# Performance work log

Measured on AMD Instinct MI355X. Metric: run time of the kernel, lower is better.

The kernel has to match this reference:

```python
import jax, jax.numpy as jnp
import numpy as np

N_NODES = 50000
N_EDGES = 800000
N_GRAPHS = 256
D = 256
L = 3
BN_EPS = 1e-5


def setup_inputs() -> dict:
    key = jax.random.key(0)
    ks = jax.random.split(key, 8)
    x = jax.random.normal(ks[0], (N_NODES, D), dtype=jnp.float32)
    edge_index = jax.random.randint(ks[1], (2, N_EDGES), 0, N_NODES, dtype=jnp.int64)
    batch = jnp.sort(jax.random.randint(ks[2], (N_NODES,), 0, N_GRAPHS, dtype=jnp.int64))
    # small init scale keeps ReLU/BN chain numerically tame
    w1 = jax.random.normal(ks[3], (L, D, D), dtype=jnp.float32) * 0.05
    b1 = jnp.zeros((L, D), dtype=jnp.float32)
    w2 = jax.random.normal(ks[4], (L, D, D), dtype=jnp.float32) * 0.05
    b2 = jnp.zeros((L, D), dtype=jnp.float32)
    gamma = jnp.ones((L, D), dtype=jnp.float32)
    beta = jnp.zeros((L, D), dtype=jnp.float32)
    return {"x": x, "edge_index": edge_index, "batch": batch,
            "w1": w1, "b1": b1, "w2": w2, "b2": b2,
            "gamma": gamma, "beta": beta}


def reference(x, edge_index, batch, w1, b1, w2, b2, gamma, beta):
    src = edge_index[0]  # message senders (x_j)
    dst = edge_index[1]  # aggregation targets (x_i)
    h = x
    xs = []
    for i in range(L):
        # GINConv (eps=0): MLP(x_i + sum_{j in N(i)} x_j)
        agg = jax.ops.segment_sum(h[src], dst, num_segments=N_NODES)  # [N, D]
        z = h + agg
        z = jnp.maximum(z @ w1[i] + b1[i], 0.0) @ w2[i] + b2[i]  # Linear-ReLU-Linear
        z = jnp.maximum(z, 0.0)  # F.relu after conv
        # BatchNorm1d (training mode: biased batch stats over nodes)
        mean = jnp.mean(z, axis=0)
        var = jnp.var(z, axis=0)
        z = (z - mean) * jax.lax.rsqrt(var + BN_EPS) * gamma[i] + beta[i]
        xs.append(z)
        h = z
    # global_add_pool per layer, then concat along features -> [G, L*D]
    pooled = [jax.ops.segment_sum(xi, batch, num_segments=N_GRAPHS) for xi in xs]
    return jnp.concatenate(pooled, axis=1)
```

## Files before the change

kernel.cpp:

```cpp
#include <hip/hip_runtime.h>

#define NN 50000
#define NE 800000
#define NG 256
#define DD 256
#define NL 3
#define BN_EPS 1e-5f
#define MPAD 50048
#define CAP 96
#define NMB 391

typedef short bf16x8 __attribute__((ext_vector_type(8)));
typedef float f32x4 __attribute__((ext_vector_type(4)));
typedef unsigned short ushort8 __attribute__((ext_vector_type(8)));

__device__ __forceinline__ unsigned short f2bf(float f) {
    unsigned int u = __float_as_uint(f);
    u += 0x7FFFu + ((u >> 16) & 1u);
    return (unsigned short)(u >> 16);
}
__device__ __forceinline__ float bf2f(unsigned short s) {
    return __uint_as_float(((unsigned int)s) << 16);
}

#define R0 3200000
#define R1 393216
#define R2 50000
#define R3 12288
#define R4 256
#define R5 256
#define RTOT (R0 + R1 + R2 + R3 + R4 + R5)

__global__ void k_setup(const float* __restrict__ x, const float* __restrict__ w1,
                        const float* __restrict__ w2, const int* __restrict__ batch,
                        unsigned short* __restrict__ hbf, unsigned short* __restrict__ wt,
                        int* __restrict__ deg, unsigned short* __restrict__ zbf,
                        int* __restrict__ gstart) {
    int i = blockIdx.x * blockDim.x + threadIdx.x;
    if (i < R0) {
        float4 v = ((const float4*)x)[i];
        ushort4 o;
        o.x = f2bf(v.x); o.y = f2bf(v.y); o.z = f2bf(v.z); o.w = f2bf(v.w);
        ((ushort4*)hbf)[i] = o;
        return;
    }
    i -= R0;
    if (i < R1) {
        int mat = i >> 16;
        int n = (i >> 8) & 255;
        int k = i & 255;
        const float* src = (mat < 3) ? (w1 + ((size_t)mat << 16)) : (w2 + ((size_t)(mat - 3) << 16));
        wt[i] = f2bf(src[k * 256 + n]);
        return;
    }
    i -= R1;
    if (i < R2) { deg[i] = 0; return; }
    i -= R2;
    if (i < R3) { zbf[NN * DD + i] = 0; return; }
    i -= R3;
    if (i < R4) { hbf[(size_t)NN * DD + i] = 0; return; }
    i -= R4;
    if (i < R5) {
        int g = i;
        int lo = 0, hi = NN;
        while (lo < hi) {
            int mid = (lo + hi) >> 1;
            if (batch[mid] < g) lo = mid + 1; else hi = mid;
        }
        gstart[g] = lo;
        if (g == 0) gstart[NG] = NN;
    }
}

__global__ void k_scatter(const int* __restrict__ ei, int* __restrict__ deg,
                          unsigned short* __restrict__ elist) {
    int e = blockIdx.x * blockDim.x + threadIdx.x;
    if (e >= NE) return;
    int s = ei[e];
    int d = ei[NE + e];
    int pos = atomicAdd(&deg[d], 1);
    elist[(size_t)d * CAP + pos] = (unsigned short)s;
}

template<int HALF>
__global__ __launch_bounds__(256) void k_agg_bf(const unsigned short* __restrict__ h,
                                                const int* __restrict__ deg,
                                                const unsigned short* __restrict__ elist,
                                                unsigned short* __restrict__ z0) {
    int wave = threadIdx.x >> 6;
    int lane = threadIdx.x & 63;
    int node = blockIdx.x * 4 + wave;
    int chunk = lane & 15;
    int eway = lane >> 4;
    const int base = HALF * 16 + chunk;
    const ushort8* h8 = (const ushort8*)h;

    float acc[8];
    if (eway == 0) {
        ushort8 own = h8[(size_t)node * 32 + base];
        #pragma unroll
        for (int j = 0; j < 8; ++j) acc[j] = bf2f(own[j]);
    } else {
        #pragma unroll
        for (int j = 0; j < 8; ++j) acc[j] = 0.f;
    }

    int n = deg[node];
    const unsigned short* el = elist + (size_t)node * CAP;
    int i = 0;
    for (; i + 8 <= n; i += 8) {
        ushort8 sv = *(const ushort8*)(el + i);
        int i0 = sv[eway];
        int i1 = sv[eway + 4];
        ushort8 r0 = h8[(size_t)i0 * 32 + base];
        ushort8 r1 = h8[(size_t)i1 * 32 + base];
        #pragma unroll
        for (int j = 0; j < 8; ++j) acc[j] += bf2f(r0[j]);
        #pragma unroll
        for (int j = 0; j < 8; ++j) acc[j] += bf2f(r1[j]);
    }
    for (; i < n; i += 4) {
        int e = i + eway;
        int idx = (e < n) ? (int)el[e] : NN;
        ushort8 r = h8[(size_t)idx * 32 + base];
        #pragma unroll
        for (int j = 0; j < 8; ++j) acc[j] += bf2f(r[j]);
    }

    ushort8 o;
    #pragma unroll
    for (int j = 0; j < 8; ++j) {
        float v = acc[j];
        v += __shfl_xor(v, 16);
        v += __shfl_xor(v, 32);
        o[j] = f2bf(v);
    }
    if (eway == 0) ((ushort8*)z0)[(size_t)node * 32 + base] = o;
}

__global__ __launch_bounds__(512, 2) void k_mlp(const unsigned short* __restrict__ A,
                                                const unsigned short* __restrict__ BT1,
                                                const unsigned short* __restrict__ BT2,
                                                const float* __restrict__ b1,
                                                const float* __restrict__ b2,
                                                float* __restrict__ Cout,
                                                float* __restrict__ pstat) {
    __shared__ short As[128 * 64];
    __shared__ short Bs[256 * 64];
    __shared__ short H1[128 * 256];
    __shared__ float spart[2][256][2];
    int tid = threadIdx.x;
    int lane = tid & 63;
    int wave = tid >> 6;
    int wr = wave >> 2, wc = wave & 3;
    long m0 = (long)blockIdx.x * 128;
    const int r = lane & 15, hi = lane >> 4;

    f32x4 acc[4][4];
    #pragma unroll
    for (int m = 0; m < 4; ++m)
        #pragma unroll
        for (int n = 0; n < 4; ++n)
            acc[m][n] = (f32x4){0.f, 0.f, 0.f, 0.f};

    for (int k0 = 0; k0 < DD; k0 += 64) {
        #pragma unroll
        for (int p = 0; p < 2; ++p) {
            int flat = p * 512 + tid;
            int row = flat >> 3, c8 = flat & 7;
            int slot = c8 ^ (row & 7);
            *(bf16x8*)(As + row * 64 + slot * 8) =
                *(const bf16x8*)(A + (m0 + row) * DD + k0 + c8 * 8);
        }
        #pragma unroll
        for (int p = 0; p < 4; ++p) {
            int flat = p * 512 + tid;
            int row = flat >> 3, c8 = flat & 7;
            int slot = c8 ^ (row & 7);
            *(bf16x8*)(Bs + row * 64 + slot * 8) =
                *(const bf16x8*)(BT1 + (long)row * DD + k0 + c8 * 8);
        }
        __syncthreads();
        bf16x8 af[4][2], bfr[4][2];
        #pragma unroll
        for (int m = 0; m < 4; ++m) {
            int row = wr * 64 + m * 16 + r;
            #pragma unroll
            for (int kk = 0; kk < 2; ++kk) {
                int slot = (kk * 4 + hi) ^ (row & 7);
                af[m][kk] = *(const bf16x8*)(As + row * 64 + slot * 8);
            }
        }
        #pragma unroll
        for (int n = 0; n < 4; ++n) {
            int col = wc * 64 + n * 16 + r;
            #pragma unroll
            for (int kk = 0; kk < 2; ++kk) {
                int slot = (kk * 4 + hi) ^ (col & 7);
                bfr[n][kk] = *(const bf16x8*)(Bs + col * 64 + slot * 8);
            }
        }
        #pragma unroll
        for (int kk = 0; kk < 2; ++kk)
            #pragma unroll
            for (int m = 0; m < 4; ++m)
                #pragma unroll
                for (int n = 0; n < 4; ++n)
                    acc[m][n] = __builtin_amdgcn_mfma_f32_16x16x32_bf16(af[m][kk], bfr[n][kk], acc[m][n], 0, 0, 0);
        __syncthreads();
    }

    #pragma unroll
    for (int n = 0; n < 4; ++n) {
        int col = wc * 64 + n * 16 + r;
        float bv = b1[col];
        int g = col >> 3, j8 = col & 7;
        #pragma unroll
        for (int m = 0; m < 4; ++m) {
            #pragma unroll
            for (int j = 0; j < 4; ++j) {
                int row = wr * 64 + m * 16 + hi * 4 + j;
                float v = acc[m][n][j] + bv;
                v = v > 0.f ? v : 0.f;
                H1[row * 256 + (g ^ (row & 7)) * 8 + j8] = (short)f2bf(v);
            }
        }
    }
    #pragma unroll
    for (int m = 0; m < 4; ++m)
        #pragma unroll
        for (int n = 0; n < 4; ++n)
            acc[m][n] = (f32x4){0.f, 0.f, 0.f, 0.f};
    __syncthreads();

    for (int k0 = 0; k0 < DD; k0 += 64) {
        #pragma unroll
        for (int p = 0; p < 4; ++p) {
            int flat = p * 512 + tid;
            int row = flat >> 3, c8 = flat & 7;
            int slot = c8 ^ (row & 7);
            *(bf16x8*)(Bs + row * 64 + slot * 8) =
                *(const bf16x8*)(BT2 + (long)row * DD + k0 + c8 * 8);
        }
        __syncthreads();
        bf16x8 af[4][2], bfr[4][2];
        #pragma unroll
        for (int m = 0; m < 4; ++m) {
            int row = wr * 64 + m * 16 + r;
            #pragma unroll
            for (int kk = 0; kk < 2; ++kk) {
                int g = (k0 >> 3) + kk * 4 + hi;
                af[m][kk] = *(const bf16x8*)(H1 + row * 256 + (g ^ (row & 7)) * 8);
            }
        }
        #pragma unroll
        for (int n = 0; n < 4; ++n) {
            int col = wc * 64 + n * 16 + r;
            #pragma unroll
            for (int kk = 0; kk < 2; ++kk) {
                int slot = (kk * 4 + hi) ^ (col & 7);
                bfr[n][kk] = *(const bf16x8*)(Bs + col * 64 + slot * 8);
            }
        }
        #pragma unroll
        for (int kk = 0; kk < 2; ++kk)
            #pragma unroll
            for (int m = 0; m < 4; ++m)
                #pragma unroll
                for (int n = 0; n < 4; ++n)
                    acc[m][n] = __builtin_amdgcn_mfma_f32_16x16x32_bf16(af[m][kk], bfr[n][kk], acc[m][n], 0, 0, 0);
        __syncthreads();
    }

    #pragma unroll
    for (int n = 0; n < 4; ++n) {
        int col = wc * 64 + n * 16 + r;
        float bv = b2[col];
        float cs = 0.f, cs2 = 0.f;
        #pragma unroll
        for (int m = 0; m < 4; ++m) {
            #pragma unroll
            for (int j = 0; j < 4; ++j) {
                long grow = m0 + wr * 64 + m * 16 + hi * 4 + j;
                float v = acc[m][n][j] + bv;
                v = v > 0.f ? v : 0.f;
                Cout[grow * DD + col] = v;
                float vm = (grow < NN) ? v : 0.f;
                cs += vm; cs2 += vm * vm;
            }
        }
        cs  += __shfl_xor(cs, 16);  cs  += __shfl_xor(cs, 32);
        cs2 += __shfl_xor(cs2, 16); cs2 += __shfl_xor(cs2, 32);
        if (hi == 0) {
            spart[wr][col][0] = cs;
            spart[wr][col][1] = cs2;
        }
    }
    __syncthreads();
    if (tid < 256) {
        float s  = spart[0][tid][0] + spart[1][tid][0];
        float s2 = spart[0][tid][1] + spart[1][tid][1];
        pstat[(size_t)blockIdx.x * 512 + tid] = s;
        pstat[(size_t)blockIdx.x * 512 + 256 + tid] = s2;
    }
}

__global__ __launch_bounds__(256) void k_bnscale2(const float* __restrict__ pstat,
                                                  const float* __restrict__ gamma,
                                                  const float* __restrict__ beta,
                                                  float* __restrict__ ss) {
    int c = blockIdx.x;
    int t = threadIdx.x;
    float s = 0.f, s2 = 0.f;
    for (int mb = t; mb < NMB; mb += 256) {
        s  += pstat[(size_t)mb * 512 + c];
        s2 += pstat[(size_t)mb * 512 + 256 + c];
    }
    __shared__ float rs[256], rs2[256];
    rs[t] = s; rs2[t] = s2;
    __syncthreads();
    #pragma unroll
    for (int d = 128; d > 0; d >>= 1) {
        if (t < d) { rs[t] += rs[t + d]; rs2[t] += rs2[t + d]; }
        __syncthreads();
    }
    if (t == 0) {
        float mean = rs[0] * (1.0f / NN);
        float var = rs2[0] * (1.0f / NN) - mean * mean;
        float sc = gamma[c] * rsqrtf(var + BN_EPS);
        ss[c] = sc;
        ss[DD + c] = beta[c] - mean * sc;
    }
}

template<int LAST>
__global__ __launch_bounds__(512) void k_bnpool(const float* __restrict__ z,
                                                const float* __restrict__ ss,
                                                const int* __restrict__ gstart,
                                                unsigned short* __restrict__ hbf,
                                                float* __restrict__ out, int layer) {
    __shared__ float4 red[16][32];
    int g = blockIdx.x;
    int ch = blockIdx.y;
    int t = threadIdx.x;
    int q = t & 31, rg = t >> 5;
    int cq = ch * 32 + q;
    float4 sc = ((const float4*)ss)[cq];
    float4 sh = ((const float4*)(ss + DD))[cq];
    int lo = gstart[g], hi = gstart[g + 1];
    float4 s = {0.f, 0.f, 0.f, 0.f};
    const float4* z4 = (const float4*)z;
    ushort4* h4 = (ushort4*)hbf;
    for (int r = lo + rg; r < hi; r += 16) {
        float4 v = z4[(size_t)r * 64 + cq];
        v.x = v.x * sc.x + sh.x;
        v.y = v.y * sc.y + sh.y;
        v.z = v.z * sc.z + sh.z;
        v.w = v.w * sc.w + sh.w;
        s.x += v.x; s.y += v.y; s.z += v.z; s.w += v.w;
        if (!LAST) {
            ushort4 o;
            o.x = f2bf(v.x); o.y = f2bf(v.y); o.z = f2bf(v.z); o.w = f2bf(v.w);
            h4[(size_t)r * 64 + cq] = o;
        }
    }
    red[rg][q] = s;
    __syncthreads();
    #pragma unroll
    for (int d = 8; d > 0; d >>= 1) {
        if (rg < d) {
            float4 a = red[rg][q], b = red[rg + d][q];
            a.x += b.x; a.y += b.y; a.z += b.z; a.w += b.w;
            red[rg][q] = a;
        }
        __syncthreads();
    }
    if (rg == 0) {
        ((float4*)(out + (size_t)g * (NL * DD) + layer * DD))[cq] = red[0][q];
    }
}

extern "C" void kernel_launch(void* const* d_in, const int* in_sizes, int n_in,
                              void* d_out, int out_size, void* d_ws, size_t ws_size,
                              hipStream_t stream) {
    const float* x     = (const float*)d_in[0];
    const int*   ei    = (const int*)d_in[1];
    const int*   batch = (const int*)d_in[2];
    const float* w1    = (const float*)d_in[3];
    const float* b1    = (const float*)d_in[4];
    const float* w2    = (const float*)d_in[5];
    const float* b2    = (const float*)d_in[6];
    const float* gamma = (const float*)d_in[7];
    const float* beta  = (const float*)d_in[8];
    float* out = (float*)d_out;

    char* ws = (char*)d_ws;
    size_t off = 0;
    auto alloc = [&](size_t bytes) -> void* {
        void* p = ws + off;
        off += (bytes + 255) & ~size_t(255);
        return p;
    };
    float*          buf0 = (float*)alloc((size_t)MPAD * DD * 4);
    unsigned short* zbf  = (unsigned short*)alloc((size_t)MPAD * DD * 2);
    unsigned short* hbf  = (unsigned short*)alloc((size_t)(NN + 64) * DD * 2);
    unsigned short* wt   = (unsigned short*)alloc((size_t)6 * DD * DD * 2);
    int* deg    = (int*)alloc((size_t)NN * 4);
    unsigned short* elist = (unsigned short*)alloc((size_t)NN * CAP * 2);
    int* gstart = (int*)alloc((size_t)(NG + 1) * 4);
    float* pstat = (float*)alloc((size_t)NMB * 512 * 4);
    float* ss   = (float*)alloc(2 * DD * 4);

    k_setup<<<(RTOT + 255) / 256, 256, 0, stream>>>(x, w1, w2, batch, hbf, wt, deg, zbf, gstart);
    k_scatter<<<(NE + 255) / 256, 256, 0, stream>>>(ei, deg, elist);

    for (int l = 0; l < NL; ++l) {
        k_agg_bf<0><<<NN / 4, 256, 0, stream>>>(hbf, deg, elist, zbf);
        k_agg_bf<1><<<NN / 4, 256, 0, stream>>>(hbf, deg, elist, zbf);
        k_mlp<<<NMB, 512, 0, stream>>>(zbf, wt + (size_t)l * DD * DD,
                                       wt + (size_t)(3 + l) * DD * DD,
                                       b1 + l * DD, b2 + l * DD, buf0, pstat);
        k_bnscale2<<<DD, 256, 0, stream>>>(pstat, gamma + l * DD, beta + l * DD, ss);
        if (l < NL - 1)
            k_bnpool<0><<<dim3(NG, 2), 512, 0, stream>>>(buf0, ss, gstart, hbf, out, l);
        else
            k_bnpool<1><<<dim3(NG, 2), 512, 0, stream>>>(buf0, ss, gstart, hbf, out, l);
    }
}
```

Before: 416.5 us.

## Bin edges by destination block and merge aggregation halves into one kernel

Replaces the global-atomic edge scatter with a three-pass binning scheme: histogram destinations into 256-node bins, scan, write packed edges into bins, then build per-node edge lists using shared-memory atomics. This is meant to cut contended global atomics and scattered writes. The aggregation also becomes a single launch covering the full 256-wide row, with two half-waves each taking alternate edges, instead of two launches over 128-column halves. The price is extra kernels and a binbuf buffer. Each wave now processes twice the row width per edge, so every gather fetches whole rows.

```diff
diff --git a/kernel.cpp b/kernel.cpp
--- a/kernel.cpp
+++ b/kernel.cpp
@@ -9,6 +9,7 @@
 #define MPAD 50048
 #define CAP 96
 #define NMB 391
+#define NBIN 196
 
 typedef short bf16x8 __attribute__((ext_vector_type(8)));
 typedef float f32x4 __attribute__((ext_vector_type(4)));
@@ -25,17 +26,17 @@
 
 #define R0 3200000
 #define R1 393216
-#define R2 50000
-#define R3 12288
+#define R2 12288
+#define R3 256
 #define R4 256
-#define R5 256
+#define R5 NBIN
 #define RTOT (R0 + R1 + R2 + R3 + R4 + R5)
 
 __global__ void k_setup(const float* __restrict__ x, const float* __restrict__ w1,
                         const float* __restrict__ w2, const int* __restrict__ batch,
                         unsigned short* __restrict__ hbf, unsigned short* __restrict__ wt,
-                        int* __restrict__ deg, unsigned short* __restrict__ zbf,
-                        int* __restrict__ gstart) {
+                        unsigned short* __restrict__ zbf, int* __restrict__ gstart,
+                        int* __restrict__ bin_cnt) {
     int i = blockIdx.x * blockDim.x + threadIdx.x;
     if (i < R0) {
         float4 v = ((const float4*)x)[i];
@@ -54,13 +55,11 @@
         return;
     }
     i -= R1;
-    if (i < R2) { deg[i] = 0; return; }
+    if (i < R2) { zbf[NN * DD + i] = 0; return; }
     i -= R2;
-    if (i < R3) { zbf[NN * DD + i] = 0; return; }
+    if (i < R3) { hbf[(size_t)NN * DD + i] = 0; return; }
     i -= R3;
-    if (i < R4) { hbf[(size_t)NN * DD + i] = 0; return; }
-    i -= R4;
-    if (i < R5) {
+    if (i < R4) {
         int g = i;
         int lo = 0, hi = NN;
         while (lo < hi) {
@@ -69,20 +68,99 @@
         }
         gstart[g] = lo;
         if (g == 0) gstart[NG] = NN;
-    }
-}
-
-__global__ void k_scatter(const int* __restrict__ ei, int* __restrict__ deg,
-                          unsigned short* __restrict__ elist) {
-    int e = blockIdx.x * blockDim.x + threadIdx.x;
-    if (e >= NE) return;
-    int s = ei[e];
-    int d = ei[NE + e];
-    int pos = atomicAdd(&deg[d], 1);
-    elist[(size_t)d * CAP + pos] = (unsigned short)s;
-}
-
-template<int HALF>
+        return;
+    }
+    i -= R4;
+    if (i < R5) bin_cnt[i] = 0;
+}
+
+__global__ __launch_bounds__(256) void k_bin1(const int* __restrict__ ei,
+                                              int* __restrict__ bin_cnt) {
+    __shared__ int hist[NBIN];
+    int t = threadIdx.x;
+    for (int i = t; i < NBIN; i += 256) hist[i] = 0;
+    __syncthreads();
+    #pragma unroll
+    for (int j = 0; j < 4; ++j) {
+        int e = blockIdx.x * 1024 + j * 256 + t;
+        if (e < NE) atomicAdd(&hist[ei[NE + e] >> 8], 1);
+    }
+    __syncthreads();
+    for (int i = t; i < NBIN; i += 256)
+        if (hist[i]) atomicAdd(&bin_cnt[i], hist[i]);
+}
+
+__global__ void k_binscan(const int* __restrict__ bin_cnt, int* __restrict__ bin_start,
+                          int* __restrict__ bin_cursor) {
+    __shared__ int s[256];
+    int t = threadIdx.x;
+    int v = (t < NBIN) ? bin_cnt[t] : 0;
+    s[t] = v;
+    __syncthreads();
+    #pragma unroll
+    for (int d = 1; d < 256; d <<= 1) {
+        int a = (t >= d) ? s[t - d] : 0;
+        __syncthreads();
+        s[t] += a;
+        __syncthreads();
+    }
+    int excl = s[t] - v;
+    if (t < NBIN) { bin_start[t] = excl; bin_cursor[t] = excl; }
+    if (t == 0) bin_start[NBIN] = NE;
+}
+
+__global__ __launch_bounds__(256) void k_bin2(const int* __restrict__ ei,
+                                              int* __restrict__ bin_cursor,
+                                              unsigned int* __restrict__ binbuf) {
+    __shared__ int hist[NBIN], base[NBIN], lcur[NBIN];
+    int t = threadIdx.x;
+    for (int i = t; i < NBIN; i += 256) { hist[i] = 0; lcur[i] = 0; }
+    __syncthreads();
+    int d[4], s[4];
+    #pragma unroll
+    for (int j = 0; j < 4; ++j) {
+        int e = blockIdx.x * 1024 + j * 256 + t;
+        if (e < NE) {
+            s[j] = ei[e];
+            d[j] = ei[NE + e];
+            atomicAdd(&hist[d[j] >> 8], 1);
+        } else d[j] = -1;
+    }
+    __syncthreads();
+    for (int i = t; i < NBIN; i += 256)
+        base[i] = hist[i] ? atomicAdd(&bin_cursor[i], hist[i]) : 0;
+    __syncthreads();
+    #pragma unroll
+    for (int j = 0; j < 4; ++j) {
+        if (d[j] >= 0) {
+            int b = d[j] >> 8;
+            int o = atomicAdd(&lcur[b], 1);
+            binbuf[base[b] + o] = (unsigned)s[j] | ((unsigned)(d[j] & 255) << 16);
+        }
+    }
+}
+
+__global__ __launch_bounds__(256) void k_bin3(const unsigned int* __restrict__ binbuf,
+                                              const int* __restrict__ bin_start,
+                                              unsigned short* __restrict__ elist,
+                                              int* __restrict__ deg) {
+    __shared__ int ldeg[256];
+    int b = blockIdx.x, t = threadIdx.x;
+    ldeg[t] = 0;
+    __syncthreads();
+    int lo = bin_start[b], hi = bin_start[b + 1];
+    for (int i = lo + t; i < hi; i += 256) {
+        unsigned v = binbuf[i];
+        int src = v & 0xFFFF;
+        int dl = v >> 16;
+        int pos = atomicAdd(&ldeg[dl], 1);
+        elist[(size_t)(b * 256 + dl) * CAP + pos] = (unsigned short)src;
+    }
+    __syncthreads();
+    int node = b * 256 + t;
+    if (node < NN) deg[node] = ldeg[t];
+}
+
 __global__ __launch_bounds__(256) void k_agg_bf(const unsigned short* __restrict__ h,
                                                 const int* __restrict__ deg,
                                                 const unsigned short* __restrict__ elist,
@@ -90,14 +168,13 @@
     int wave = threadIdx.x >> 6;
     int lane = threadIdx.x & 63;
     int node = blockIdx.x * 4 + wave;
-    int chunk = lane & 15;
-    int eway = lane >> 4;
-    const int base = HALF * 16 + chunk;
+    int chunk = lane & 31;
+    int half = lane >> 5;
     const ushort8* h8 = (const ushort8*)h;
 
     float acc[8];
-    if (eway == 0) {
-        ushort8 own = h8[(size_t)node * 32 + base];
+    if (half == 0) {
+        ushort8 own = h8[(size_t)node * 32 + chunk];
         #pragma unroll
         for (int j = 0; j < 8; ++j) acc[j] = bf2f(own[j]);
     } else {
@@ -110,19 +187,28 @@
     int i = 0;
     for (; i + 8 <= n; i += 8) {
         ushort8 sv = *(const ushort8*)(el + i);
-        int i0 = sv[eway];
-        int i1 = sv[eway + 4];
-        ushort8 r0 = h8[(size_t)i0 * 32 + base];
-        ushort8 r1 = h8[(size_t)i1 * 32 + base];
+        int i0 = half ? sv[1] : sv[0];
+        int i1 = half ? sv[3] : sv[2];
+        int i2 = half ? sv[5] : sv[4];
+        int i3 = half ? sv[7] : sv[6];
+        ushort8 r0 = h8[(size_t)i0 * 32 + chunk];
+        ushort8 r1 = h8[(size_t)i1 * 32 + chunk];
+        ushort8 r2 = h8[(size_t)i2 * 32 + chunk];
+        ushort8 r3 = h8[(size_t)i3 * 32 + chunk];
         #pragma unroll
         for (int j = 0; j < 8; ++j) acc[j] += bf2f(r0[j]);
         #pragma unroll
         for (int j = 0; j < 8; ++j) acc[j] += bf2f(r1[j]);
-    }
-    for (; i < n; i += 4) {
-        int e = i + eway;
-        int idx = (e < n) ? (int)el[e] : NN;
-        ushort8 r = h8[(size_t)idx * 32 + base];
+        #pragma unroll
+        for (int j = 0; j < 8; ++j) acc[j] += bf2f(r2[j]);
+        #pragma unroll
+        for (int j = 0; j < 8; ++j) acc[j] += bf2f(r3[j]);
+    }
+    for (; i < n; i += 2) {
+        int s0 = el[i];
+        int s1 = (i + 1 < n) ? (int)el[i + 1] : NN;
+        int idx = half ? s1 : s0;
+        ushort8 r = h8[(size_t)idx * 32 + chunk];
         #pragma unroll
         for (int j = 0; j < 8; ++j) acc[j] += bf2f(r[j]);
     }
@@ -130,12 +216,10 @@
     ushort8 o;
     #pragma unroll
     for (int j = 0; j < 8; ++j) {
-        float v = acc[j];
-        v += __shfl_xor(v, 16);
-        v += __shfl_xor(v, 32);
-        o[j] = f2bf(v);
-    }
-    if (eway == 0) ((ushort8*)z0)[(size_t)node * 32 + base] = o;
+        float other = __shfl_xor(acc[j], 32);
+        o[j] = f2bf(acc[j] + other);
+    }
+    if (half == 0) ((ushort8*)z0)[(size_t)node * 32 + chunk] = o;
 }
 
 __global__ __launch_bounds__(512, 2) void k_mlp(const unsigned short* __restrict__ A,
@@ -407,16 +491,23 @@
     unsigned short* wt   = (unsigned short*)alloc((size_t)6 * DD * DD * 2);
     int* deg    = (int*)alloc((size_t)NN * 4);
     unsigned short* elist = (unsigned short*)alloc((size_t)NN * CAP * 2);
+    unsigned int* binbuf = (unsigned int*)alloc((size_t)NE * 4);
+    int* bin_cnt    = (int*)alloc(NBIN * 4);
+    int* bin_start  = (int*)alloc((NBIN + 1) * 4);
+    int* bin_cursor = (int*)alloc(NBIN * 4);
     int* gstart = (int*)alloc((size_t)(NG + 1) * 4);
     float* pstat = (float*)alloc((size_t)NMB * 512 * 4);
     float* ss   = (float*)alloc(2 * DD * 4);
 
-    k_setup<<<(RTOT + 255) / 256, 256, 0, stream>>>(x, w1, w2, batch, hbf, wt, deg, zbf, gstart);
-    k_scatter<<<(NE + 255) / 256, 256, 0, stream>>>(ei, deg, elist);
+    k_setup<<<(RTOT + 255) / 256, 256, 0, stream>>>(x, w1, w2, batch, hbf, wt, zbf, gstart, bin_cnt);
+    const int EB = (NE + 1023) / 1024;
+    k_bin1<<<EB, 256, 0, stream>>>(ei, bin_cnt);
+    k_binscan<<<1, 256, 0, stream>>>(bin_cnt, bin_start, bin_cursor);
+    k_bin2<<<EB, 256, 0, stream>>>(ei, bin_cursor, binbuf);
+    k_bin3<<<NBIN, 256, 0, stream>>>(binbuf, bin_start, elist, deg);
 
     for (int l = 0; l < NL; ++l) {
-        k_agg_bf<0><<<NN / 4, 256, 0, stream>>>(hbf, deg, elist, zbf);
-        k_agg_bf<1><<<NN / 4, 256, 0, stream>>>(hbf, deg, elist, zbf);
+        k_agg_bf<<<NN / 4, 256, 0, stream>>>(hbf, deg, elist, zbf);
         k_mlp<<<NMB, 512, 0, stream>>>(zbf, wt + (size_t)l * DD * DD,
                                        wt + (size_t)(3 + l) * DD * DD,
                                        b1 + l * DD, b2 + l * DD, buf0, pstat);
```

Result: faster. 395.4 us (-5.1%).
